# Kernel optimization log

Measured on AMD Instinct MI355X. Metric: run time of the kernel, lower is better.

The kernel has to match this reference:

```python
import jax, jax.numpy as jnp
import numpy as np

K = 10  # knn neighbors
EPS = 1e-5  # BatchNorm eps


def mish(x):
    # x * tanh(softplus(x)), numerically stable softplus
    return x * jnp.tanh(jnp.logaddexp(x, 0.0))


def bn(x, g, b, m, v, nd):
    # inference-mode BatchNorm over channel axis 1
    shp = (1, -1) + (1,) * (nd - 2)
    scale = g.reshape(shp) / jnp.sqrt(v.reshape(shp) + EPS)
    return (x - m.reshape(shp)) * scale + b.reshape(shp)


def graph_feature(x, k):
    # x: [B, C, N] -> edge features [B, 2C, N, k]
    xt = jnp.swapaxes(x, 1, 2)  # [B, N, C]
    sq = jnp.sum(x * x, axis=1)  # [B, N]
    # negative squared pairwise distance [B, N, N]
    neg = 2.0 * jnp.einsum('bcn,bcm->bnm', x, x) - sq[:, :, None] - sq[:, None, :]
    idx = jax.lax.top_k(neg, k)[1]  # [B, N, k] nearest-neighbor indices
    nbr = jax.vmap(lambda a, i: a[i])(xt, idx)  # [B, N, k, C]
    ctr = jnp.broadcast_to(xt[:, :, None, :], nbr.shape)
    feat = jnp.concatenate([nbr - ctr, ctr], axis=-1)  # [B, N, k, 2C]
    return jnp.transpose(feat, (0, 3, 1, 2))  # [B, 2C, N, k]


def c2(w, x):  # 1x1 Conv2d
    return jnp.einsum('oc,bcnk->bonk', w, x)


def c1(w, x):  # 1x1 Conv1d
    return jnp.einsum('oc,bcn->bon', w, x)


def setup_inputs() -> dict:
    key = jax.random.key(0)
    ks = jax.random.split(key, 32)
    B, d, N = 8, 3, 2048
    emb, nb = 1024, 6
    def w(k_, o, c):
        return jax.random.normal(k_, (o, c), dtype=jnp.float32) * (1.0 / np.sqrt(c))
    inp = {
        'x': jax.random.normal(ks[0], (B, d, N), dtype=jnp.float32),
        'w1': w(ks[1], 64, 2 * d), 'w2': w(ks[2], 64, 64),
        'w3': w(ks[3], 64, 128), 'w4': w(ks[4], 64, 64),
        'w5': w(ks[5], 64, 128), 'w6': w(ks[6], emb, 192),
        'w7': w(ks[7], 512, emb + 192), 'w8': w(ks[8], 256, 512),
        'w9': w(ks[9], d * nb, 256),
        'g15': jax.random.uniform(ks[10], (5, 64), jnp.float32, 0.5, 1.5),
        'b15': jax.random.normal(ks[11], (5, 64), jnp.float32) * 0.1,
        'm15': jax.random.normal(ks[12], (5, 64), jnp.float32) * 0.1,
        'v15': jax.random.uniform(ks[13], (5, 64), jnp.float32, 0.5, 1.5),
        'g6': jax.random.uniform(ks[14], (emb,), jnp.float32, 0.5, 1.5),
        'b6': jax.random.normal(ks[15], (emb,), jnp.float32) * 0.1,
        'm6': jax.random.normal(ks[16], (emb,), jnp.float32) * 0.1,
        'v6': jax.random.uniform(ks[17], (emb,), jnp.float32, 0.5, 1.5),
        'g7': jax.random.uniform(ks[18], (512,), jnp.float32, 0.5, 1.5),
        'b7': jax.random.normal(ks[19], (512,), jnp.float32) * 0.1,
        'm7': jax.random.normal(ks[20], (512,), jnp.float32) * 0.1,
        'v7': jax.random.uniform(ks[21], (512,), jnp.float32, 0.5, 1.5),
        'g8': jax.random.uniform(ks[22], (256,), jnp.float32, 0.5, 1.5),
        'b8': jax.random.normal(ks[23], (256,), jnp.float32) * 0.1,
        'm8': jax.random.normal(ks[24], (256,), jnp.float32) * 0.1,
        'v8': jax.random.uniform(ks[25], (256,), jnp.float32, 0.5, 1.5),
    }
    return inp


def reference(x, w1, w2, w3, w4, w5, w6, w7, w8, w9,
              g15, b15, m15, v15, g6, b6, m6, v6,
              g7, b7, m7, v7, g8, b8, m8, v8):
    N = x.shape[2]
    f = graph_feature(x, K)                                   # [B, 6, N, K]
    h = mish(bn(c2(w1, f), g15[0], b15[0], m15[0], v15[0], 4))
    h = mish(bn(c2(w2, h), g15[1], b15[1], m15[1], v15[1], 4))
    x1 = jnp.max(h, axis=-1)                                  # [B, 64, N]
    f = graph_feature(x1, K)
    h = mish(bn(c2(w3, f), g15[2], b15[2], m15[2], v15[2], 4))
    h = mish(bn(c2(w4, h), g15[3], b15[3], m15[3], v15[3], 4))
    x2 = jnp.max(h, axis=-1)
    f = graph_feature(x2, K)
    h = mish(bn(c2(w5, f), g15[4], b15[4], m15[4], v15[4], 4))
    x3 = jnp.max(h, axis=-1)
    cat = jnp.concatenate([x1, x2, x3], axis=1)               # [B, 192, N]
    h6 = mish(bn(c1(w6, cat), g6, b6, m6, v6, 3))             # [B, emb, N]
    glob = jnp.max(h6, axis=-1, keepdims=True)
    glob = jnp.broadcast_to(glob, (glob.shape[0], glob.shape[1], N))
    h = jnp.concatenate([glob, cat], axis=1)                  # [B, emb+192, N]
    h = mish(bn(c1(w7, h), g7, b7, m7, v7, 3))
    h = mish(bn(c1(w8, h), g8, b8, m8, v8, 3))
    return c1(w9, h)                                          # [B, 18, N]
```

## Files before the change

kernel.cpp:

```cpp
#include <hip/hip_runtime.h>
#include <math.h>

#define BN_EPS 1e-5f
typedef unsigned long long u64;
typedef __attribute__((ext_vector_type(8))) short bf16x8;
typedef __attribute__((ext_vector_type(8))) unsigned short u16x8;
typedef __attribute__((ext_vector_type(4))) float f32x4;

__device__ __forceinline__ float mishf(float x){
  float u = __expf(fminf(x, 20.f));
  float w = u * (u + 2.f);
  return x * w / (w + 2.f);
}

__device__ __forceinline__ unsigned fenc(float f){
  unsigned u = __float_as_uint(f);
  return u ^ ((unsigned)((int)u >> 31) | 0x80000000u);
}
__device__ __forceinline__ float fdec(unsigned e){
  unsigned u = (e & 0x80000000u) ? (e & 0x7fffffffu) : ~e;
  return __uint_as_float(u);
}

__device__ __forceinline__ void bfsplit(float a, unsigned short &h, unsigned short &l){
  unsigned u = __float_as_uint(a);
  unsigned hb = (u + 0x7FFFu + ((u >> 16) & 1u)) >> 16;
  h = (unsigned short)hb;
  float hf = __uint_as_float(hb << 16);
  float r = a - hf;
  unsigned v = __float_as_uint(r);
  l = (unsigned short)((v + 0x7FFFu + ((v >> 16) & 1u)) >> 16);
}

__device__ __forceinline__ u64 mkkey(float v, int i){
  return ((u64)fenc(v) << 32) | (unsigned)(~i);
}
__device__ __forceinline__ int keyidx(u64 k){ return (int)(~(unsigned)k); }

__device__ __forceinline__ void ins10k(u64 (&L)[10], u64 k){
  if (k <= L[9]) return;
  #pragma unroll
  for (int p = 9; p >= 1; --p)
    L[p] = (k > L[p-1]) ? L[p-1] : ((k > L[p]) ? k : L[p]);
  L[0] = (k > L[0]) ? k : L[0];
}

#define TOPK_INIT(S, I, eth) do { \
  _Pragma("unroll") \
  for (int _j = 0; _j < 10; ++_j) { S[_j] = 0x007FFFFFu; I[_j] = 0x7fffffffu; } \
  eth = 0x007FFFFFu; } while (0)

__device__ __forceinline__ void topk_push32(unsigned (&S)[10], unsigned (&I)[10],
                                            unsigned &eth, float v, unsigned i){
  unsigned e = fenc(v);
  if (e > eth) {
    #pragma unroll
    for (int p = 9; p >= 1; --p) {
      bool gp = e > S[p-1];
      bool gc = e > S[p];
      I[p] = gp ? I[p-1] : (gc ? i : I[p]);
      unsigned ns;
      asm("v_med3_u32 %0, %1, %2, %3" : "=v"(ns) : "v"(e), "v"(S[p-1]), "v"(S[p]));
      S[p] = ns;
    }
    bool g0 = e > S[0];
    I[0] = g0 ? i : I[0];
    S[0] = g0 ? e : S[0];
    eth = S[9];
  }
}
#define KSENT mkkey(-INFINITY, 0x7fffffff)

__global__ void k_diag(float* __restrict__ out, float v){ out[0] = v; }

__global__ __launch_bounds__(256)
void k_zero(unsigned* __restrict__ p){
  p[blockIdx.x * 256 + threadIdx.x] = 0u;
}

__global__ __launch_bounds__(256)
void k_knn3(const float* __restrict__ x, int* __restrict__ idxout){
  __shared__ __align__(16) char smem[33024];
  float4* pts4 = (float4*)smem;
  u64* m1 = (u64*)smem;
  u64* m2 = (u64*)(smem + 20480);
  const int t  = threadIdx.x;
  const int b  = blockIdx.x >> 7;
  const int p0 = (blockIdx.x & 127) * 16;
  const int pt = t & 15, ch = t >> 4;
  const float* xb = x + (size_t)b * 6144;

  for (int i = t; i < 2048; i += 256) {
    float x0 = xb[i], x1 = xb[2048 + i], x2 = xb[4096 + i];
    float s2 = x0 * x0; s2 = fmaf(x1, x1, s2); s2 = fmaf(x2, x2, s2);
    pts4[(i >> 7) * 129 + (i & 127)] = make_float4(x0, x1, x2, s2);
  }
  __syncthreads();

  const int g = p0 + pt;
  const float4 ov = pts4[(g >> 7) * 129 + (g & 127)];
  unsigned S[10], I[10], eth;
  TOPK_INIT(S, I, eth);
  const float4* cp = pts4 + ch * 129;
  #pragma unroll 4
  for (int j = 0; j < 128; ++j) {
    float4 pv = cp[j];
    float dot = ov.x * pv.x; dot = fmaf(ov.y, pv.y, dot); dot = fmaf(ov.z, pv.z, dot);
    float key = fmaf(2.f, dot, -ov.w) - pv.w;
    topk_push32(S, I, eth, key, ch * 128 + j);
  }
  __syncthreads();

  #pragma unroll
  for (int j = 0; j < 10; ++j)
    m1[(ch * 10 + j) * 16 + pt] = ((u64)S[j] << 32) | (unsigned)(~I[j]);
  __syncthreads();

  if (t < 64) {
    int p1 = t >> 2, q = t & 3;
    u64 F[10];
    #pragma unroll
    for (int j = 0; j < 10; ++j) F[j] = KSENT;
    for (int c2 = 0; c2 < 4; ++c2) {
      int cch = q * 4 + c2;
      #pragma unroll
      for (int j = 0; j < 10; ++j)
        ins10k(F, m1[(cch * 10 + j) * 16 + p1]);
    }
    #pragma unroll
    for (int j = 0; j < 10; ++j)
      m2[(q * 10 + j) * 16 + p1] = F[j];
  }
  __syncthreads();

  if (t < 16) {
    u64 F[10];
    #pragma unroll
    for (int j = 0; j < 10; ++j) F[j] = KSENT;
    for (int q = 0; q < 4; ++q)
      #pragma unroll
      for (int j = 0; j < 10; ++j)
        ins10k(F, m2[(q * 10 + j) * 16 + t]);
    #pragma unroll
    for (int j = 0; j < 10; ++j)
      idxout[(size_t)(b * 2048 + p0 + t) * 10 + j] = keyidx(F[j]);
  }
}

__global__ __launch_bounds__(256)
void k_knn2p(const unsigned short* __restrict__ H, const unsigned short* __restrict__ Lp,
             const float* __restrict__ sq, u64* __restrict__ pk){
  __shared__ __align__(16) char smem[20480];
  float* ssB = (float*)smem;
  u64*   mg  = (u64*)smem;

  const int t  = threadIdx.x;
  const int bx = blockIdx.x;
  const int cc = bx & 7;
  const int rg = (bx >> 3) & 31;
  const int b  = bx >> 8;
  const int p0 = rg * 64;
  const int c0 = cc * 256;
  const int lane = t & 63, w = t >> 6;
  const int la  = (lane & 15) * 8;
  const int sub = lane >> 4;
  const int qrow = w * 16 + (lane & 15);
  const int rt = t % 10;

  const size_t ag = ((size_t)((b * 2048 + p0) >> 4) + w) * 8 + sub;
  bf16x8 aH0 = *(const bf16x8*)&H [ ag      * 128 + la];
  bf16x8 aL0 = *(const bf16x8*)&Lp[ ag      * 128 + la];
  bf16x8 aH1 = *(const bf16x8*)&H [(ag + 4) * 128 + la];
  bf16x8 aL1 = *(const bf16x8*)&Lp[(ag + 4) * 128 + la];

  ssB[t] = sq[b * 2048 + c0 + (t & 255)];
  const float nsA = -sq[b * 2048 + p0 + qrow];

  unsigned S[10], I[10], eth;
  TOPK_INIT(S, I, eth);
  __syncthreads();

  for (int m0 = 0; m0 < 256; m0 += 64) {
    const size_t cgb = ((size_t)((b * 2048 + c0 + m0) >> 4)) * 8 + sub;
    #pragma unroll
    for (int tile = 0; tile < 4; ++tile) {
      const size_t cg = (cgb + (size_t)tile * 8) * 128 + la;
      bf16x8 bH0 = *(const bf16x8*)&H [cg];
      bf16x8 bL0 = *(const bf16x8*)&Lp[cg];
      bf16x8 bH1 = *(const bf16x8*)&H [cg + 512];
      bf16x8 bL1 = *(const bf16x8*)&Lp[cg + 512];
      f32x4 acc = {0.f, 0.f, 0.f, 0.f};
      acc = __builtin_amdgcn_mfma_f32_16x16x32_bf16(bH0, aL0, acc, 0, 0, 0);
      acc = __builtin_amdgcn_mfma_f32_16x16x32_bf16(bL0, aH0, acc, 0, 0, 0);
      acc = __builtin_amdgcn_mfma_f32_16x16x32_bf16(bH0, aH0, acc, 0, 0, 0);
      acc = __builtin_amdgcn_mfma_f32_16x16x32_bf16(bH1, aL1, acc, 0, 0, 0);
      acc = __builtin_amdgcn_mfma_f32_16x16x32_bf16(bL1, aH1, acc, 0, 0, 0);
      acc = __builtin_amdgcn_mfma_f32_16x16x32_bf16(bH1, aH1, acc, 0, 0, 0);
      float4 s4 = *(const float4*)&ssB[m0 + tile * 16 + sub * 4];
      int cbase = c0 + m0 + tile * 16 + sub * 4;
      topk_push32(S, I, eth, fmaf(2.f, acc[0], nsA) - s4.x, cbase);
      topk_push32(S, I, eth, fmaf(2.f, acc[1], nsA) - s4.y, cbase + 1);
      topk_push32(S, I, eth, fmaf(2.f, acc[2], nsA) - s4.z, cbase + 2);
      topk_push32(S, I, eth, fmaf(2.f, acc[3], nsA) - s4.w, cbase + 3);
    }
  }
  __syncthreads();

  #pragma unroll
  for (int j = 0; j < 10; ++j) {
    int rj = j + rt; rj = (rj >= 10) ? rj - 10 : rj;
    mg[(qrow * 4 + sub) * 10 + rj] = ((u64)S[j] << 32) | (unsigned)(~I[j]);
  }
  __syncthreads();
  if (t < 64) {
    u64 F[10];
    #pragma unroll
    for (int j = 0; j < 10; ++j) F[j] = KSENT;
    for (int c2 = 0; c2 < 4; ++c2)
      #pragma unroll
      for (int j = 0; j < 10; ++j) {
        int rj = j + rt; rj = (rj >= 10) ? rj - 10 : rj;
        ins10k(F, mg[(t * 4 + c2) * 10 + rj]);
      }
    size_t base = (size_t)(b * 2048 + p0 + t) * 80 + cc * 10;
    #pragma unroll
    for (int j = 0; j < 10; ++j) pk[base + j] = F[j];
  }
}

__global__ __launch_bounds__(64)
void k_kmerge(const u64* __restrict__ pk, int* __restrict__ idxout){
  int row = blockIdx.x * 64 + threadIdx.x;
  u64 F[10];
  #pragma unroll
  for (int j = 0; j < 10; ++j) F[j] = KSENT;
  size_t base = (size_t)row * 80;
  for (int e = 0; e < 80; ++e) ins10k(F, pk[base + e]);
  #pragma unroll
  for (int j = 0; j < 10; ++j) idxout[(size_t)row * 10 + j] = keyidx(F[j]);
}

__global__ __launch_bounds__(256)
void k_uv3(const float* __restrict__ x, const float* __restrict__ w1,
           const float* __restrict__ gg, const float* __restrict__ vv,
           float* __restrict__ UV){
  int i = blockIdx.x * 256 + threadIdx.x;
  int p = i >> 6, o = i & 63;
  int b = p >> 11, n = p & 2047;
  float s = gg[o] / sqrtf(vv[o] + BN_EPS);
  const float* xb = x + (size_t)b * 6144 + n;
  float x0 = xb[0], x1 = xb[2048], x2 = xb[4096];
  const float* wr = w1 + o * 6;
  float u = s * (wr[0] * x0 + wr[1] * x1 + wr[2] * x2);
  float v = s * ((wr[3] - wr[0]) * x0 + (wr[4] - wr[1]) * x1 + (wr[5] - wr[2]) * x2);
  UV[(size_t)p * 128 + o] = u;
  UV[(size_t)p * 128 + 64 + o] = v;
}

__global__ __launch_bounds__(256)
void k_uv(const float* __restrict__ A, int lda, int aoff,
          const float* __restrict__ w,
          const float* __restrict__ gg, const float* __restrict__ vv,
          float* __restrict__ UV){
  __shared__ float As[16][68];
  __shared__ float Bs[16][68];
  __shared__ float ss[64];
  const int t = threadIdx.x;
  const int tx = t & 15, ty = t >> 4;
  const int m0 = blockIdx.x * 64;
  const int half = blockIdx.y;
  if (t < 64) ss[t] = gg[t] / sqrtf(vv[t] + BN_EPS);
  __syncthreads();
  float acc[4][4] = {};
  for (int k0 = 0; k0 < 64; k0 += 16) {
    for (int i = t; i < 1024; i += 256) {
      int m = i >> 4, k = i & 15;
      As[k][m] = A[(size_t)(m0 + m) * lda + aoff + k0 + k];
    }
    for (int i = t; i < 1024; i += 256) {
      int n = i >> 4, k = i & 15;
      int kk = k0 + k;
      float wv = half ? (w[n * 128 + 64 + kk] - w[n * 128 + kk]) : w[n * 128 + kk];
      Bs[k][n] = wv * ss[n];
    }
    __syncthreads();
    #pragma unroll
    for (int k = 0; k < 16; ++k) {
      float4 a4 = *(const float4*)&As[k][tx * 4];
      float4 b4 = *(const float4*)&Bs[k][ty * 4];
      float am[4] = {a4.x, a4.y, a4.z, a4.w};
      float bm[4] = {b4.x, b4.y, b4.z, b4.w};
      #pragma unroll
      for (int q = 0; q < 4; ++q)
        #pragma unroll
        for (int r = 0; r < 4; ++r)
          acc[q][r] = fmaf(am[q], bm[r], acc[q][r]);
    }
    __syncthreads();
  }
  #pragma unroll
  for (int q = 0; q < 4; ++q)
    #pragma unroll
    for (int r = 0; r < 4; ++r)
      UV[(size_t)(m0 + tx * 4 + q) * 128 + half * 64 + ty * 4 + r] = acc[q][r];
}

__global__ __launch_bounds__(256)
void k_edge2(const float* __restrict__ UV, const int* __restrict__ idx,
             const float* __restrict__ w2,
             const float* __restrict__ g1, const float* __restrict__ b1,
             const float* __restrict__ m1, const float* __restrict__ v1,
             const float* __restrict__ g2, const float* __restrict__ b2,
             const float* __restrict__ m2, const float* __restrict__ v2,
             float* __restrict__ cat, int coff,
             unsigned short* __restrict__ kH, unsigned short* __restrict__ kL,
             float* __restrict__ sqout){
  __shared__ float Ha[64][81];
  __shared__ float Ws[64][68];
  __shared__ float o1s[64], s2s[64], o2s[64];
  __shared__ int   ejs[80];
  const int t = threadIdx.x;
  const int p0 = blockIdx.x * 8;
  const int batch = p0 >> 11;
  if (t < 80) ejs[t] = batch * 2048 + (idx[p0 * 10 + t] & 2047);
  if (t < 64) {
    float s1 = g1[t] / sqrtf(v1[t] + BN_EPS);
    o1s[t] = b1[t] - m1[t] * s1;
    float s2 = g2[t] / sqrtf(v2[t] + BN_EPS);
    s2s[t] = s2;
    o2s[t] = b2[t] - m2[t] * s2;
  }
  for (int i = t; i < 4096; i += 256) {
    int k = i & 63, n = i >> 6;
    Ws[k][n] = w2[n * 64 + k];
  }
  __syncthreads();

  for (int i = t; i < 5120; i += 256) {
    int e = i >> 6, c = i & 63;
    int p = p0 + e / 10;
    float hv = UV[(size_t)ejs[e] * 128 + c] + UV[(size_t)p * 128 + 64 + c] + o1s[c];
    Ha[c][e] = mishf(hv);
  }
  __syncthreads();

  const int tx = t & 15, ty = t >> 4;
  float acc[5][4] = {};
  #pragma unroll 8
  for (int k = 0; k < 64; ++k) {
    float av[5];
    #pragma unroll
    for (int i2 = 0; i2 < 5; ++i2) av[i2] = Ha[k][tx * 5 + i2];
    float4 b4 = *(const float4*)&Ws[k][ty * 4];
    float bv[4] = {b4.x, b4.y, b4.z, b4.w};
    #pragma unroll
    for (int i2 = 0; i2 < 5; ++i2)
      #pragma unroll
      for (int r = 0; r < 4; ++r)
        acc[i2][r] = fmaf(av[i2], bv[r], acc[i2][r]);
  }
  __syncthreads();
  #pragma unroll
  for (int i2 = 0; i2 < 5; ++i2)
    #pragma unroll
    for (int r = 0; r < 4; ++r) {
      int o = ty * 4 + r;
      Ha[o][tx * 5 + i2] = mishf(acc[i2][r] * s2s[o] + o2s[o]);
    }
  __syncthreads();

  for (int i = t; i < 512; i += 256) {
    int p = i >> 6, o = i & 63;
    float mx = Ha[o][p * 10];
    #pragma unroll
    for (int k = 1; k < 10; ++k) mx = fmaxf(mx, Ha[o][p * 10 + k]);
    cat[(size_t)(p0 + p) * 192 + coff + o] = mx;
    unsigned short hh, ll;
    bfsplit(mx, hh, ll);
    int n = p0 + p;
    size_t pos = ((size_t)(n >> 4) * 8 + (o >> 3)) * 128 + (n & 15) * 8 + (o & 7);
    kH[pos] = hh; kL[pos] = ll;
    float r = mx * mx;
    #pragma unroll
    for (int m = 32; m; m >>= 1) r += __shfl_xor(r, m);
    if (o == 0) sqout[p0 + p] = r;
  }
}

__global__ __launch_bounds__(256)
void k_edge3(const float* __restrict__ UV, const int* __restrict__ idx,
             const float* __restrict__ gg, const float* __restrict__ bb,
             const float* __restrict__ mn, const float* __restrict__ vv,
             float* __restrict__ cat){
  int i = blockIdx.x * 256 + threadIdx.x;
  int p = i >> 6, o = i & 63;
  int batch = p >> 11;
  float s = gg[o] / sqrtf(vv[o] + BN_EPS);
  float of = bb[o] - mn[o] * s;
  float v_ = UV[(size_t)p * 128 + 64 + o] + of;
  float mx = -INFINITY;
  #pragma unroll
  for (int k = 0; k < 10; ++k) {
    int j = batch * 2048 + (idx[p * 10 + k] & 2047);
    mx = fmaxf(mx, mishf(UV[(size_t)j * 128 + o] + v_));
  }
  cat[(size_t)p * 192 + 128 + o] = mx;
}

__global__ __launch_bounds__(256)
void k_split(const float* __restrict__ src, int ld, int koff, int K,
             unsigned short* __restrict__ H, unsigned short* __restrict__ L){
  int i = blockIdx.x * 256 + threadIdx.x;
  int kg = K >> 3;
  int n = i / kg, g = i - n * kg;
  const float* s = &src[(size_t)n * ld + koff + g * 8];
  float4 v0 = *(const float4*)s, v1 = *(const float4*)(s + 4);
  float vv[8] = {v0.x, v0.y, v0.z, v0.w, v1.x, v1.y, v1.z, v1.w};
  u16x8 hh, ll;
  #pragma unroll
  for (int q = 0; q < 8; ++q) {
    unsigned short h_, l_;
    bfsplit(vv[q], h_, l_);
    hh[q] = h_; ll[q] = l_;
  }
  size_t pos = ((size_t)(n >> 4) * kg + g) * 128 + (n & 15) * 8;
  *(u16x8*)&H[pos] = hh;
  *(u16x8*)&L[pos] = ll;
}

#define EP_BNMISH      0
#define EP_MAXGLOB     1
#define EP_BIAS_BNMISH 2

template<int EPI>
__global__ __launch_bounds__(256)
void k_gemm(const unsigned short* __restrict__ APH, const unsigned short* __restrict__ APL,
            const unsigned short* __restrict__ WPH, const unsigned short* __restrict__ WPL,
            int K,
            const float* __restrict__ gg, const float* __restrict__ bb,
            const float* __restrict__ mn, const float* __restrict__ vv,
            const float* __restrict__ bias,
            float* __restrict__ out, int ldo,
            unsigned short* __restrict__ oH, unsigned short* __restrict__ oL, int oldo,
            unsigned* __restrict__ glob)
{
  __shared__ float red[64][17];
  const int t = threadIdx.x;
  const int lane = t & 63, w = t >> 6;
  const int m0 = blockIdx.x * 64, n0 = blockIdx.y * 64;
  const int kg = K >> 3;
  const int la = (lane & 15) * 8;
  f32x4 acc[4] = {{0,0,0,0},{0,0,0,0},{0,0,0,0},{0,0,0,0}};
  const size_t abase = ((size_t)((m0 >> 4) + w) * kg + (lane >> 4)) * 128 + la;

  for (int k0 = 0; k0 < K; k0 += 32) {
    size_t ao = abase + (size_t)(k0 >> 3) * 128;
    bf16x8 aH = *(const bf16x8*)&APH[ao];
    bf16x8 aL = *(const bf16x8*)&APL[ao];
    #pragma unroll
    for (int tt = 0; tt < 4; ++tt) {
      size_t wo = ((size_t)((n0 >> 4) + tt) * kg + (k0 >> 3) + (lane >> 4)) * 128 + la;
      bf16x8 bH = *(const bf16x8*)&WPH[wo];
      bf16x8 bL = *(const bf16x8*)&WPL[wo];
      acc[tt] = __builtin_amdgcn_mfma_f32_16x16x32_bf16(aL, bH, acc[tt], 0, 0, 0);
      acc[tt] = __builtin_amdgcn_mfma_f32_16x16x32_bf16(aH, bL, acc[tt], 0, 0, 0);
      acc[tt] = __builtin_amdgcn_mfma_f32_16x16x32_bf16(aH, bH, acc[tt], 0, 0, 0);
    }
  }

  const int mrow = m0 + w * 16 + ((lane >> 4) << 2);
  const int batch = m0 >> 11;

  if (EPI == EP_MAXGLOB) {
    #pragma unroll
    for (int tt = 0; tt < 4; ++tt) {
      int nn = n0 + tt * 16 + (lane & 15);
      float s = gg[nn] / sqrtf(vv[nn] + BN_EPS);
      float f = bb[nn] - mn[nn] * s;
      float mx = -INFINITY;
      #pragma unroll
      for (int r = 0; r < 4; ++r) mx = fmaxf(mx, mishf(acc[tt][r] * s + f));
      red[tt * 16 + (lane & 15)][w * 4 + (lane >> 4)] = mx;
    }
    __syncthreads();
    if (t < 64) {
      float v = red[t][0];
      #pragma unroll
      for (int q = 1; q < 16; ++q) v = fmaxf(v, red[t][q]);
      atomicMax(&glob[batch * 1024 + n0 + t], fenc(v));
    }
  } else {
    #pragma unroll
    for (int tt = 0; tt < 4; ++tt) {
      int nn = n0 + tt * 16 + (lane & 15);
      float s = gg[nn] / sqrtf(vv[nn] + BN_EPS);
      float f = bb[nn] - mn[nn] * s;
      float bv = (EPI == EP_BIAS_BNMISH) ? bias[batch * 512 + nn] : 0.f;
      #pragma unroll
      for (int r = 0; r < 4; ++r) {
        int m = mrow + r;
        float h = mishf((acc[tt][r] + bv) * s + f);
        if (EPI == EP_BIAS_BNMISH) {
          unsigned short hh, ll;
          bfsplit(h, hh, ll);
          size_t pos = ((size_t)(m >> 4) * (oldo >> 3) + (nn >> 3)) * 128
                       + (m & 15) * 8 + (nn & 7);
          oH[pos] = hh; oL[pos] = ll;
        } else {
          out[(size_t)m * ldo + nn] = h;
        }
      }
    }
  }
}

__global__ __launch_bounds__(256)
void k_t7(const unsigned* __restrict__ glob, const float* __restrict__ w7,
          float* __restrict__ t7){
  int i = blockIdx.x * 256 + threadIdx.x;
  int b = i >> 9, o = i & 511;
  float acc = 0.f;
  for (int c = 0; c < 1024; ++c)
    acc = fmaf(w7[(size_t)o * 1216 + c], fdec(glob[b * 1024 + c]), acc);
  t7[i] = acc;
}

__global__ __launch_bounds__(256)
void k_out(const float* __restrict__ h8, const float* __restrict__ w9,
           float* __restrict__ out)
{
  __shared__ float row[4][256];
  const int t = threadIdx.x;
  const int g = t >> 6, l = t & 63;
  const int p = blockIdx.x * 4 + g;
  for (int c = l; c < 256; c += 64)
    row[g][c] = h8[(size_t)p * 256 + c];
  __syncthreads();
  if (l < 18) {
    float acc = 0.f;
    for (int c = 0; c < 256; ++c)
      acc = fmaf(row[g][c], w9[l * 256 + c], acc);
    int b = p >> 11, n = p & 2047;
    out[(size_t)b * 36864 + l * 2048 + n] = acc;
  }
}

extern "C" void kernel_launch(void* const* d_in, const int* in_sizes, int n_in,
                              void* d_out, int out_size, void* d_ws, size_t ws_size,
                              hipStream_t stream)
{
  const size_t OFF_IDX  = 262144;
  const size_t OFF_CAT  = 917504;
  const size_t OFF_GLOB = 13500416;
  const size_t OFF_T7   = 13533184;
  const size_t OFF_H7   = 13549568;
  const size_t OFF_KNN  = OFF_H7 + 8388608;
  const size_t OFF_H8   = 47104000;
  const size_t NEED     = 63881216;

  static const int EXP[26] = {
    49152, 384, 4096, 8192, 4096, 8192, 196608, 622592, 131072, 4608,
    320, 320, 320, 320, 1024, 1024, 1024, 1024,
    512, 512, 512, 512, 256, 256, 256, 256 };
  if (n_in < 26) { k_diag<<<1,1,0,stream>>>((float*)d_out, 16384.f); return; }
  for (int i = 0; i < 26; ++i)
    if (in_sizes[i] != EXP[i]) {
      k_diag<<<1,1,0,stream>>>((float*)d_out, 4096.f + 128.f * i); return;
    }
  if (out_size != 294912) { k_diag<<<1,1,0,stream>>>((float*)d_out, 20480.f); return; }
  if (ws_size < NEED) {
    k_diag<<<1,1,0,stream>>>((float*)d_out, 24576.f + (float)(ws_size >> 20)); return;
  }

  const float* x  = (const float*)d_in[0];
  const float* w1 = (const float*)d_in[1];
  const float* w2 = (const float*)d_in[2];
  const float* w3 = (const float*)d_in[3];
  const float* w4 = (const float*)d_in[4];
  const float* w5 = (const float*)d_in[5];
  const float* w6 = (const float*)d_in[6];
  const float* w7 = (const float*)d_in[7];
  const float* w8 = (const float*)d_in[8];
  const float* w9 = (const float*)d_in[9];
  const float* g15 = (const float*)d_in[10];
  const float* b15 = (const float*)d_in[11];
  const float* m15 = (const float*)d_in[12];
  const float* v15 = (const float*)d_in[13];
  const float* g6 = (const float*)d_in[14];
  const float* b6 = (const float*)d_in[15];
  const float* m6 = (const float*)d_in[16];
  const float* v6 = (const float*)d_in[17];
  const float* g7 = (const float*)d_in[18];
  const float* b7 = (const float*)d_in[19];
  const float* m7 = (const float*)d_in[20];
  const float* v7 = (const float*)d_in[21];
  const float* g8 = (const float*)d_in[22];
  const float* b8 = (const float*)d_in[23];
  const float* m8 = (const float*)d_in[24];
  const float* v8 = (const float*)d_in[25];

  char* ws = (char*)d_ws;
  int*      idx  = (int*)(ws + OFF_IDX);
  float*    cat  = (float*)(ws + OFF_CAT);
  unsigned* glob = (unsigned*)(ws + OFF_GLOB);
  float*    t7   = (float*)(ws + OFF_T7);
  float*    UV   = (float*)(ws + OFF_H7);
  float*    h8   = (float*)(ws + OFF_H8);
  float*    sq   = (float*)(ws + OFF_H8);
  u64*      pk   = (u64*)(ws + OFF_H8 + 65536);
  unsigned short* knnH = (unsigned short*)(ws + OFF_KNN);
  unsigned short* knnL = (unsigned short*)(ws + OFF_KNN + 2097152);

  unsigned short* catH = (unsigned short*)(ws + OFF_H8);
  unsigned short* catL = (unsigned short*)(ws + OFF_H8 + 6291456);
  unsigned short* h7H  = (unsigned short*)(ws + OFF_H7);
  unsigned short* h7L  = (unsigned short*)(ws + OFF_H7 + 16777216);
  unsigned short* w6H  = (unsigned short*)(ws + OFF_CAT);
  unsigned short* w6L  = (unsigned short*)(ws + OFF_CAT + 393216);
  unsigned short* w7H  = (unsigned short*)(ws + OFF_CAT + 786432);
  unsigned short* w7L  = (unsigned short*)(ws + OFF_CAT + 983040);
  unsigned short* w8H  = (unsigned short*)(ws + OFF_CAT + 1179648);
  unsigned short* w8L  = (unsigned short*)(ws + OFF_CAT + 1441792);

  k_zero<<<32, 256, 0, stream>>>(glob);

  k_knn3<<<1024, 256, 0, stream>>>(x, idx);
  k_uv3<<<4096, 256, 0, stream>>>(x, w1, g15 + 0, v15 + 0, UV);
  k_edge2<<<2048, 256, 0, stream>>>(UV, idx, w2,
      g15 + 0,  b15 + 0,  m15 + 0,  v15 + 0,
      g15 + 64, b15 + 64, m15 + 64, v15 + 64, cat, 0, knnH, knnL, sq);

  k_knn2p<<<2048, 256, 0, stream>>>(knnH, knnL, sq, pk);
  k_kmerge<<<256, 64, 0, stream>>>(pk, idx);
  dim3 guv(256, 2);
  k_uv<<<guv, 256, 0, stream>>>(cat, 192, 0, w3, g15 + 128, v15 + 128, UV);
  k_edge2<<<2048, 256, 0, stream>>>(UV, idx, w4,
      g15 + 128, b15 + 128, m15 + 128, v15 + 128,
      g15 + 192, b15 + 192, m15 + 192, v15 + 192, cat, 64, knnH, knnL, sq);

  k_knn2p<<<2048, 256, 0, stream>>>(knnH, knnL, sq, pk);
  k_kmerge<<<256, 64, 0, stream>>>(pk, idx);
  k_uv<<<guv, 256, 0, stream>>>(cat, 192, 64, w5, g15 + 256, v15 + 256, UV);
  k_edge3<<<4096, 256, 0, stream>>>(UV, idx,
      g15 + 256, b15 + 256, m15 + 256, v15 + 256, cat);

  k_split<<<1536, 256, 0, stream>>>(cat, 192, 0, 192, catH, catL);
  k_split<<<96, 256, 0, stream>>>(w6, 192, 0, 192, w6H, w6L);
  k_split<<<48, 256, 0, stream>>>(w7, 1216, 1024, 192, w7H, w7L);
  k_split<<<64, 256, 0, stream>>>(w8, 512, 0, 512, w8H, w8L);

  dim3 g6g(256, 16);
  k_gemm<EP_MAXGLOB><<<g6g, 256, 0, stream>>>(
      catH, catL, w6H, w6L, 192, g6, b6, m6, v6,
      nullptr, nullptr, 0, nullptr, nullptr, 0, glob);
  k_t7<<<16, 256, 0, stream>>>(glob, w7, t7);
  dim3 g7g(256, 8);
  k_gemm<EP_BIAS_BNMISH><<<g7g, 256, 0, stream>>>(
      catH, catL, w7H, w7L, 192, g7, b7, m7, v7,
      t7, nullptr, 0, h7H, h7L, 512, nullptr);
  dim3 g8g(256, 4);
  k_gemm<EP_BNMISH><<<g8g, 256, 0, stream>>>(
      h7H, h7L, w8H, w8L, 512, g8, b8, m8, v8,
      nullptr, h8, 256, nullptr, nullptr, 0, nullptr);
  k_out<<<4096, 256, 0, stream>>>(h8, w9, (float*)d_out);
}
```

Measured before the change: 666.1 us.

## Use value-only top-k pass then threshold rescan to recover kNN indices

The first-layer kNN kernel now runs a branchless value-only top-10 insertion (med3 chain without index tracking) to find each point's 10th-best distance threshold. A second pass recomputes all distances from global memory, collects candidates at or above the threshold into a small shared buffer via atomics, and sorts them with indices. This removes the per-insert index bookkeeping, but adds a second full distance scan with global loads. Ties beyond 16 candidates are truncated, and the second pass reloads x instead of reading shared memory, which was overwritten.

```diff
diff --git a/kernel.cpp b/kernel.cpp
--- a/kernel.cpp
+++ b/kernel.cpp
@@ -45,6 +45,16 @@
   L[0] = (k > L[0]) ? k : L[0];
 }
 
+__device__ __forceinline__ void ins10s(unsigned (&S)[10], unsigned e){
+  #pragma unroll
+  for (int p = 9; p >= 1; --p){
+    unsigned ns;
+    asm("v_med3_u32 %0, %1, %2, %3" : "=v"(ns) : "v"(e), "v"(S[p-1]), "v"(S[p]));
+    S[p] = ns;
+  }
+  S[0] = (e > S[0]) ? e : S[0];
+}
+
 #define TOPK_INIT(S, I, eth) do { \
   _Pragma("unroll") \
   for (int _j = 0; _j < 10; ++_j) { S[_j] = 0x007FFFFFu; I[_j] = 0x7fffffffu; } \
@@ -81,9 +91,12 @@
 __global__ __launch_bounds__(256)
 void k_knn3(const float* __restrict__ x, int* __restrict__ idxout){
   __shared__ __align__(16) char smem[33024];
-  float4* pts4 = (float4*)smem;
-  u64* m1 = (u64*)smem;
-  u64* m2 = (u64*)(smem + 20480);
+  float4* pts4   = (float4*)smem;
+  unsigned* m1u  = (unsigned*)smem;
+  unsigned* m2u  = (unsigned*)(smem + 10240);
+  unsigned* thr  = (unsigned*)(smem + 12800);
+  int*      cnt  = (int*)(smem + 12864);
+  u64*      buf  = (u64*)(smem + 12928);
   const int t  = threadIdx.x;
   const int b  = blockIdx.x >> 7;
   const int p0 = (blockIdx.x & 127) * 16;
@@ -99,48 +112,73 @@
 
   const int g = p0 + pt;
   const float4 ov = pts4[(g >> 7) * 129 + (g & 127)];
-  unsigned S[10], I[10], eth;
-  TOPK_INIT(S, I, eth);
+  unsigned S[10];
+  #pragma unroll
+  for (int j = 0; j < 10; ++j) S[j] = 0x007FFFFFu;
   const float4* cp = pts4 + ch * 129;
   #pragma unroll 4
   for (int j = 0; j < 128; ++j) {
     float4 pv = cp[j];
     float dot = ov.x * pv.x; dot = fmaf(ov.y, pv.y, dot); dot = fmaf(ov.z, pv.z, dot);
     float key = fmaf(2.f, dot, -ov.w) - pv.w;
-    topk_push32(S, I, eth, key, ch * 128 + j);
+    ins10s(S, fenc(key));
   }
   __syncthreads();
 
   #pragma unroll
   for (int j = 0; j < 10; ++j)
-    m1[(ch * 10 + j) * 16 + pt] = ((u64)S[j] << 32) | (unsigned)(~I[j]);
+    m1u[(ch * 10 + j) * 16 + pt] = S[j];
   __syncthreads();
 
   if (t < 64) {
     int p1 = t >> 2, q = t & 3;
-    u64 F[10];
-    #pragma unroll
-    for (int j = 0; j < 10; ++j) F[j] = KSENT;
-    for (int c2 = 0; c2 < 4; ++c2) {
-      int cch = q * 4 + c2;
+    unsigned F[10];
+    #pragma unroll
+    for (int j = 0; j < 10; ++j) F[j] = 0x007FFFFFu;
+    for (int c2 = 0; c2 < 4; ++c2)
       #pragma unroll
       for (int j = 0; j < 10; ++j)
-        ins10k(F, m1[(cch * 10 + j) * 16 + p1]);
-    }
+        ins10s(F, m1u[((q * 4 + c2) * 10 + j) * 16 + p1]);
     #pragma unroll
     for (int j = 0; j < 10; ++j)
-      m2[(q * 10 + j) * 16 + p1] = F[j];
+      m2u[(q * 10 + j) * 16 + p1] = F[j];
   }
   __syncthreads();
 
   if (t < 16) {
-    u64 F[10];
-    #pragma unroll
-    for (int j = 0; j < 10; ++j) F[j] = KSENT;
+    unsigned F[10];
+    #pragma unroll
+    for (int j = 0; j < 10; ++j) F[j] = 0x007FFFFFu;
     for (int q = 0; q < 4; ++q)
       #pragma unroll
       for (int j = 0; j < 10; ++j)
-        ins10k(F, m2[(q * 10 + j) * 16 + t]);
+        ins10s(F, m2u[(q * 10 + j) * 16 + t]);
+    thr[t] = F[9];
+    cnt[t] = 0;
+  }
+  __syncthreads();
+
+  const unsigned th = thr[pt];
+  for (int j = 0; j < 128; ++j) {
+    int c = ch * 128 + j;
+    float x0 = xb[c], x1 = xb[2048 + c], x2 = xb[4096 + c];
+    float s2 = x0 * x0; s2 = fmaf(x1, x1, s2); s2 = fmaf(x2, x2, s2);
+    float dot = ov.x * x0; dot = fmaf(ov.y, x1, dot); dot = fmaf(ov.z, x2, dot);
+    float key = fmaf(2.f, dot, -ov.w) - s2;
+    unsigned e = fenc(key);
+    if (e >= th) {
+      int slot = atomicAdd(&cnt[pt], 1);
+      if (slot < 16) buf[pt * 16 + slot] = ((u64)e << 32) | (unsigned)(~c);
+    }
+  }
+  __syncthreads();
+
+  if (t < 16) {
+    u64 F[10];
+    #pragma unroll
+    for (int j = 0; j < 10; ++j) F[j] = KSENT;
+    int n = cnt[t]; n = (n < 16) ? n : 16;
+    for (int e2 = 0; e2 < n; ++e2) ins10k(F, buf[t * 16 + e2]);
     #pragma unroll
     for (int j = 0; j < 10; ++j)
       idxout[(size_t)(b * 2048 + p0 + t) * 10 + j] = keyidx(F[j]);
```

Result: faster. 650.6 us (-2.3%).
